# Performance work log

Hardware: AMD Instinct MI355X
Metric: run time of the kernel (lower is better)

Reference implementation:

```python
import jax, jax.numpy as jnp
import numpy as np

COMMITMENT_COST = 0.25
LAMBDA_KL = 1.0
EPS = 1e-10


def setup_inputs() -> dict:
    key = jax.random.key(0)
    k1, k2 = jax.random.split(key)
    x = jax.random.normal(k1, (8, 4096, 256), dtype=jnp.float32)
    embedding = jax.random.normal(k2, (1024, 256), dtype=jnp.float32)
    return {"x": x, "embedding": embedding}


def reference(x, embedding):
    B, T, D = x.shape
    M, _ = embedding.shape
    x_sg = jax.lax.stop_gradient(x)
    x_flat = x_sg.reshape(-1, D)  # [N, D]
    distances = (jnp.sum(embedding ** 2, axis=1)[None, :]
                 + jnp.sum(x_flat ** 2, axis=1, keepdims=True)
                 - 2.0 * (x_flat @ embedding.T))  # [N, M]
    indices = jnp.argmin(distances.astype(jnp.float32), axis=-1)  # [N]
    quantized = embedding[indices].reshape(B, T, D)
    # losses (x detached in both terms, matching torch)
    loss = (COMMITMENT_COST * jnp.mean((x_sg - quantized) ** 2)
            + jnp.mean((quantized - x_sg) ** 2)) * LAMBDA_KL
    # straight-through estimator
    quantized_st = x + jax.lax.stop_gradient(quantized - x)
    # avg of one-hot encodings == normalized code counts (avoids NxM one-hot)
    N = B * T
    counts = jnp.zeros((M,), dtype=jnp.float32).at[indices].add(1.0)
    avg_probs = counts / N
    perplexity = jnp.exp(-jnp.sum(avg_probs * jnp.log(avg_probs + EPS)))
    return (quantized_st, loss, indices.reshape(B, T), perplexity)
```

## Files before the change

### kernel.cpp

```cpp
#include <hip/hip_runtime.h>


constexpr int D = 256;
constexpr int M = 1024;
constexpr int SLICES = 4;
constexpr int CHUNK = 32;
constexpr int RPB = 512;

typedef _Float16 f16;
typedef __attribute__((ext_vector_type(4))) _Float16 f16x4;
typedef __attribute__((ext_vector_type(8))) _Float16 f16x8;
typedef __attribute__((ext_vector_type(4))) float f32x4;
typedef unsigned long long u64;
typedef unsigned int u32;

constexpr size_t WS_ENORM_F = 1028;
constexpr size_t WS_KEYS_B  = 16384;

__device__ inline u64 makekey(float v, int idx) {
    u32 b = __float_as_uint(v);
    u32 enc = (b & 0x80000000u) ? ~b : (b | 0x80000000u);
    return ((u64)enc << 32) | (u32)idx;
}

__global__ __launch_bounds__(512, 2) void vq_dist_kernel(
    const float* __restrict__ x, const float* __restrict__ e,
    u64* __restrict__ keys, float* __restrict__ ws, int groups)
{
    __shared__ ushort xH[2][CHUNK * D];
    __shared__ ushort xL[2][CHUNK * D];
    __shared__ u64    wred[8][CHUNK];

    const int tid = threadIdx.x;
    const int w  = __builtin_amdgcn_readfirstlane(tid >> 6);
    const int l  = tid & 63;
    const int lr = l & 15;
    const int q  = l >> 4;
    const int bswz = (lr & 7) << 4;

    const int slice = blockIdx.x / groups;
    const int group = blockIdx.x % groups;
    const int grow0 = group * RPB;
    const int ebase = slice * 256 + w * 32;

    f16x8 Ah[2][8], Al[2][8];
    float enR[2];
#pragma unroll
    for (int rf = 0; rf < 2; ++rf) {
        float sq = 0.f;
#pragma unroll
        for (int kk = 0; kk < 8; ++kk) {
            const float* p = e + (size_t)(ebase + rf * 16 + lr) * D + kk * 32 + q * 8;
            f32x4 a = *reinterpret_cast<const f32x4*>(p);
            f32x4 b = *reinterpret_cast<const f32x4*>(p + 4);
            f16 h0=(f16)a.x,h1=(f16)a.y,h2=(f16)a.z,h3=(f16)a.w;
            f16 h4=(f16)b.x,h5=(f16)b.y,h6=(f16)b.z,h7=(f16)b.w;
            Ah[rf][kk] = (f16x8){h0,h1,h2,h3,h4,h5,h6,h7};
            Al[rf][kk] = (f16x8){(f16)(a.x-(float)h0),(f16)(a.y-(float)h1),
                                 (f16)(a.z-(float)h2),(f16)(a.w-(float)h3),
                                 (f16)(b.x-(float)h4),(f16)(b.y-(float)h5),
                                 (f16)(b.z-(float)h6),(f16)(b.w-(float)h7)};
            sq = fmaf(a.x,a.x,fmaf(a.y,a.y,fmaf(a.z,a.z,fmaf(a.w,a.w,
                 fmaf(b.x,b.x,fmaf(b.y,b.y,fmaf(b.z,b.z,fmaf(b.w,b.w,sq))))))));
        }
        sq += __shfl_xor(sq, 16, 64);
        sq += __shfl_xor(sq, 32, 64);
        enR[rf] = sq;
    }
    float enA[2][4];
#pragma unroll
    for (int rf = 0; rf < 2; ++rf)
#pragma unroll
        for (int i = 0; i < 4; ++i)
            enA[rf][i] = __shfl(enR[rf], (l & 48) | (q * 4 + i), 64);

    float sxx = 0.f;
    f32x4 st[4];
#pragma unroll
    for (int i = 0; i < 4; ++i) {
        int f = i * 512 + tid, rr = f >> 6, c4 = f & 63;
        st[i] = *reinterpret_cast<const f32x4*>(x + (size_t)(grow0 + rr) * D + c4 * 4);
    }
    auto stage_write = [&](int nb) {
#pragma unroll
        for (int i = 0; i < 4; ++i) {
            int f = i * 512 + tid, rr = f >> 6, c4 = f & 63;
            f32x4 v = st[i];
            sxx = fmaf(v.x,v.x,fmaf(v.y,v.y,fmaf(v.z,v.z,fmaf(v.w,v.w,sxx))));
            f16 h0=(f16)v.x,h1=(f16)v.y,h2=(f16)v.z,h3=(f16)v.w;
            int byte = (rr * 512 + c4 * 8) ^ ((rr & 7) << 4);
            *reinterpret_cast<f16x4*>((char*)&xH[nb][0] + byte) = (f16x4){h0,h1,h2,h3};
            *reinterpret_cast<f16x4*>((char*)&xL[nb][0] + byte) =
                (f16x4){(f16)(v.x-(float)h0),(f16)(v.y-(float)h1),
                        (f16)(v.z-(float)h2),(f16)(v.w-(float)h3)};
        }
    };
    stage_write(0);

    const int nch = RPB / CHUNK;
    for (int c = 0; c < nch; ++c) {
        if (c + 1 < nch) {
#pragma unroll
            for (int i = 0; i < 4; ++i) {
                int f = i * 512 + tid, rr = f >> 6, c4 = f & 63;
                st[i] = *reinterpret_cast<const f32x4*>(
                    x + (size_t)(grow0 + (c + 1) * CHUNK + rr) * D + c4 * 4);
            }
        }
        __syncthreads();
        const int cb = c & 1;

        f32x4 acc[2][2];
#pragma unroll
        for (int rf = 0; rf < 2; ++rf)
#pragma unroll
            for (int cf = 0; cf < 2; ++cf) acc[rf][cf] = (f32x4){0.f,0.f,0.f,0.f};

#pragma unroll
        for (int kk = 0; kk < 8; ++kk) {
            f16x8 Bh[2], Bl[2];
#pragma unroll
            for (int cf = 0; cf < 2; ++cf) {
                int byte = ((cf * 16 + lr) * 512 + kk * 64 + q * 16) ^ bswz;
                Bh[cf] = *reinterpret_cast<const f16x8*>((const char*)&xH[cb][0] + byte);
                Bl[cf] = *reinterpret_cast<const f16x8*>((const char*)&xL[cb][0] + byte);
            }
#pragma unroll
            for (int rf = 0; rf < 2; ++rf)
#pragma unroll
                for (int cf = 0; cf < 2; ++cf) {
                    acc[rf][cf] = __builtin_amdgcn_mfma_f32_16x16x32_f16(Ah[rf][kk], Bh[cf], acc[rf][cf], 0, 0, 0);
                    acc[rf][cf] = __builtin_amdgcn_mfma_f32_16x16x32_f16(Ah[rf][kk], Bl[cf], acc[rf][cf], 0, 0, 0);
                    acc[rf][cf] = __builtin_amdgcn_mfma_f32_16x16x32_f16(Al[rf][kk], Bh[cf], acc[rf][cf], 0, 0, 0);
                }
        }

        float bV[2] = {3.4e38f, 3.4e38f};
        int   bI[2] = {0, 0};
#pragma unroll
        for (int rf = 0; rf < 2; ++rf)
#pragma unroll
            for (int i = 0; i < 4; ++i) {
                int   mi = ebase + rf * 16 + q * 4 + i;
                float en = enA[rf][i];
#pragma unroll
                for (int cf = 0; cf < 2; ++cf) {
                    float dv = fmaf(-2.f, acc[rf][cf][i], en);
                    if (dv < bV[cf]) { bV[cf] = dv; bI[cf] = mi; }
                }
            }
#pragma unroll
        for (int cf = 0; cf < 2; ++cf) {
#pragma unroll
            for (int mk = 16; mk <= 32; mk <<= 1) {
                float ov = __shfl_xor(bV[cf], mk, 64);
                int   oi = __shfl_xor(bI[cf], mk, 64);
                if (ov < bV[cf] || (ov == bV[cf] && oi < bI[cf])) { bV[cf] = ov; bI[cf] = oi; }
            }
        }
        if (q == 0) {
            wred[w][lr]      = makekey(bV[0], bI[0]);
            wred[w][16 + lr] = makekey(bV[1], bI[1]);
        }
        __syncthreads();

        if (tid < 32) {
            u64 k = wred[0][tid];
#pragma unroll
            for (int ww = 1; ww < 8; ++ww) { u64 k2 = wred[ww][tid]; k = (k2 < k) ? k2 : k; }
            atomicMin(&keys[grow0 + c * CHUNK + tid], k);
        }
        if (c + 1 < nch) stage_write((c + 1) & 1);
    }

    if (slice == 0) {
#pragma unroll
        for (int o = 32; o > 0; o >>= 1) sxx += __shfl_down(sxx, o, 64);
        if (l == 0) atomicAdd(ws, sxx);
    }
}

__global__ __launch_bounds__(256) void vq_gather_kernel(
    const float* __restrict__ e, const u64* __restrict__ keys,
    float* __restrict__ outQ, float* __restrict__ outIdx, float* __restrict__ ws)
{
    __shared__ int fidx[64];
    const int tid = threadIdx.x, row0 = blockIdx.x * 64;
    if (tid < 64) {
        u64 k = keys[row0 + tid];
        u32 enc = (u32)(k >> 32);
        u32 bits = (enc & 0x80000000u) ? (enc & 0x7fffffffu) : ~enc;
        float bv = __uint_as_float(bits);
        int idx = (int)(u32)(k & 0xffffffffu);
        fidx[tid] = idx;
        outIdx[row0 + tid] = (float)idx;
        atomicAdd(ws + 1 + idx, 1.0f);
        float s = bv;
#pragma unroll
        for (int o = 32; o > 0; o >>= 1) s += __shfl_down(s, o, 64);
        if (tid == 0) atomicAdd(ws, s);
    }
    __syncthreads();
#pragma unroll
    for (int it = 0; it < 16; ++it) {
        int f = it * 256 + tid, rr = f >> 6, c4 = f & 63;
        f32x4 v = *reinterpret_cast<const f32x4*>(e + (size_t)fidx[rr] * D + c4 * 4);
        __builtin_nontemporal_store(v, reinterpret_cast<f32x4*>(outQ + (size_t)(row0 + rr) * D + c4 * 4));
    }
}

__global__ void enorm_kernel(const float* __restrict__ e, float* __restrict__ enorm) {
    int m = blockIdx.x, l = threadIdx.x;
    const f32x4 v = *reinterpret_cast<const f32x4*>(e + m * D + l * 4);
    float s = fmaf(v.x, v.x, fmaf(v.y, v.y, fmaf(v.z, v.z, v.w * v.w)));
#pragma unroll
    for (int o = 32; o > 0; o >>= 1) s += __shfl_down(s, o, 64);
    if (l == 0) enorm[m] = s;
}

__global__ __launch_bounds__(256, 2) void vq_main_kernel(
    const float* __restrict__ x, const float* __restrict__ e,
    float* __restrict__ outQ, float* __restrict__ outIdx, float* __restrict__ ws) {
    __shared__ f32x4 xs[64][64];
    __shared__ float cval[4][64];
    __shared__ int   cidx[4][64];
    __shared__ int   fidx[64];
    const int tid = threadIdx.x, row0 = blockIdx.x * 64;
#pragma unroll
    for (int it = 0; it < 16; ++it) {
        int f = it * 256 + tid, rr = f >> 6, c4 = f & 63;
        xs[rr][c4 ^ (rr & 7)] = *reinterpret_cast<const f32x4*>(x + (row0 + rr) * D + c4 * 4);
    }
    __syncthreads();
    const int r = tid & 63, c = __builtin_amdgcn_readfirstlane(tid >> 6), sw = r & 7;
    float xnorm = 0.f;
    if (c == 0) {
        f32x4 a = (f32x4){0.f,0.f,0.f,0.f};
        for (int d4 = 0; d4 < 64; ++d4) {
            f32x4 xv = xs[r][d4 ^ sw];
            a.x = fmaf(xv.x, xv.x, a.x); a.y = fmaf(xv.y, xv.y, a.y);
            a.z = fmaf(xv.z, xv.z, a.z); a.w = fmaf(xv.w, xv.w, a.w);
        }
        xnorm = (a.x + a.y) + (a.z + a.w);
    }
    const float* __restrict__ enorm = ws + WS_ENORM_F;
    float bestVal = 3.4e38f; int bestIdx = 0;
    for (int chunk = 0; chunk < M / 32; ++chunk) {
        const int m0 = chunk * 32 + c * 8;
        f32x4 acc[8];
#pragma unroll
        for (int mi = 0; mi < 8; ++mi) acc[mi] = (f32x4){0.f,0.f,0.f,0.f};
#pragma unroll 2
        for (int d4 = 0; d4 < 64; ++d4) {
            const f32x4 xv = xs[r][d4 ^ sw];
#pragma unroll
            for (int mi = 0; mi < 8; ++mi) {
                const f32x4 ev = *reinterpret_cast<const f32x4*>(e + (m0 + mi) * D + d4 * 4);
                acc[mi].x = fmaf(xv.x, ev.x, acc[mi].x); acc[mi].y = fmaf(xv.y, ev.y, acc[mi].y);
                acc[mi].z = fmaf(xv.z, ev.z, acc[mi].z); acc[mi].w = fmaf(xv.w, ev.w, acc[mi].w);
            }
        }
#pragma unroll
        for (int mi = 0; mi < 8; ++mi) {
            float dot = (acc[mi].x + acc[mi].y) + (acc[mi].z + acc[mi].w);
            float val = enorm[m0 + mi] - 2.0f * dot;
            if (val < bestVal) { bestVal = val; bestIdx = m0 + mi; }
        }
    }
    cval[c][r] = bestVal; cidx[c][r] = bestIdx;
    __syncthreads();
    if (c == 0) {
        float bv = bestVal; int bi = bestIdx;
#pragma unroll
        for (int cc = 1; cc < 4; ++cc) {
            float v = cval[cc][r]; int i = cidx[cc][r];
            if (v < bv || (v == bv && i < bi)) { bv = v; bi = i; }
        }
        fidx[r] = bi; outIdx[row0 + r] = (float)bi;
        atomicAdd(ws + 1 + bi, 1.0f);
        float dist = bv + xnorm;
#pragma unroll
        for (int o = 32; o > 0; o >>= 1) dist += __shfl_down(dist, o, 64);
        if (r == 0) atomicAdd(ws, dist);
    }
    __syncthreads();
#pragma unroll
    for (int it = 0; it < 16; ++it) {
        int f = it * 256 + tid, rr = f >> 6, c4 = f & 63;
        *reinterpret_cast<f32x4*>(outQ + (row0 + rr) * D + c4 * 4) =
            *reinterpret_cast<const f32x4*>(e + fidx[rr] * D + c4 * 4);
    }
}

__global__ void vq_final_kernel(const float* __restrict__ ws,
                                float* __restrict__ outLoss, float* __restrict__ outPpl,
                                float invN, float invND) {
    int t = threadIdx.x;
    float p = ws[1 + t] * invN;
    float term = p * logf(p + 1e-10f);
#pragma unroll
    for (int o = 32; o > 0; o >>= 1) term += __shfl_down(term, o, 64);
    __shared__ float s[16];
    if ((t & 63) == 0) s[t >> 6] = term;
    __syncthreads();
    if (t == 0) {
        float tot = 0.f;
#pragma unroll
        for (int i = 0; i < 16; ++i) tot += s[i];
        *outPpl  = expf(-tot);
        *outLoss = 1.25f * ws[0] * invND;
    }
}

extern "C" void kernel_launch(void* const* d_in, const int* in_sizes, int n_in,
                              void* d_out, int out_size, void* d_ws, size_t ws_size,
                              hipStream_t stream) {
    const float* x = (const float*)d_in[0];
    const float* e = (const float*)d_in[1];
    const int NX = in_sizes[0];
    const int N  = NX / D;

    float* out     = (float*)d_out;
    float* outQ    = out;
    float* outLoss = out + NX;
    float* outIdx  = out + NX + 1;
    float* outPpl  = out + NX + 1 + N;
    float* ws      = (float*)d_ws;
    u64*   keys    = (u64*)((char*)d_ws + WS_KEYS_B);

    const size_t need = WS_KEYS_B + (size_t)N * 8;
    (void)hipMemsetAsync(d_ws, 0, 4100, stream);
    if (ws_size >= need && (N % RPB) == 0) {
        (void)hipMemsetAsync(keys, 0xFF, (size_t)N * 8, stream);
        const int groups = N / RPB;
        vq_dist_kernel<<<SLICES * groups, 512, 0, stream>>>(x, e, keys, ws, groups);
        vq_gather_kernel<<<N / 64, 256, 0, stream>>>(e, keys, outQ, outIdx, ws);
    } else {
        enorm_kernel<<<M, 64, 0, stream>>>(e, ws + WS_ENORM_F);
        vq_main_kernel<<<N / 64, 256, 0, stream>>>(x, e, outQ, outIdx, ws);
    }
    vq_final_kernel<<<1, 1024, 0, stream>>>(ws, outLoss, outPpl,
                                            1.0f / (float)N, 1.0f / (float)NX);
}
```

Baseline: 97.21 us.

## Fuse distance, argmin and gather with x-stationary tiles and prepacked codebook

Replaces the codebook-sliced distance kernel, the 64-bit key atomicMin buffer and the separate gather kernel with one fused kernel. In the new kernel each block keeps its 128 x rows as split-fp16 fragments in registers and streams a prepacked hi/lo fp16 codebook through double-buffered LDS using global_load_lds. A new prep kernel builds the packed codebook and its norms once per call. This removes the key memset, the atomics and a kernel launch, and the argmin is done fully in-register. The cost is that every block rereads the whole 1 MB packed codebook, and the grid is small (N/128 = 256 blocks).

Measured after the change: 93.71 us. -3.6%, faster.

```diff
diff --git a/kernel.cpp b/kernel.cpp
--- a/kernel.cpp
+++ b/kernel.cpp
@@ -3,209 +3,184 @@
 
 constexpr int D = 256;
 constexpr int M = 1024;
-constexpr int SLICES = 4;
-constexpr int CHUNK = 32;
-constexpr int RPB = 512;
 
 typedef _Float16 f16;
-typedef __attribute__((ext_vector_type(4))) _Float16 f16x4;
 typedef __attribute__((ext_vector_type(8))) _Float16 f16x8;
 typedef __attribute__((ext_vector_type(4))) float f32x4;
-typedef unsigned long long u64;
-typedef unsigned int u32;
 
 constexpr size_t WS_ENORM_F = 1028;
-constexpr size_t WS_KEYS_B  = 16384;
-
-__device__ inline u64 makekey(float v, int idx) {
-    u32 b = __float_as_uint(v);
-    u32 enc = (b & 0x80000000u) ? ~b : (b | 0x80000000u);
-    return ((u64)enc << 32) | (u32)idx;
-}
-
-__global__ __launch_bounds__(512, 2) void vq_dist_kernel(
+constexpr size_t WS_TAB_B   = 8320;
+constexpr size_t WS_NEEDED  = 1056896;
+
+__device__ inline void gload_lds16(const void* g, void* l) {
+    __builtin_amdgcn_global_load_lds(
+        (const __attribute__((address_space(1))) unsigned int*)(g),
+        (__attribute__((address_space(3))) unsigned int*)(l), 16, 0, 0);
+}
+
+__global__ __launch_bounds__(256) void prep_kernel(const float* __restrict__ e,
+                                                   float* __restrict__ ws) {
+    const int b = blockIdx.x, t = threadIdx.x;
+    if (b < 256) {
+        int v    = b * 256 + t;
+        int lane = v & 63, unit = v >> 6;
+        int rf = unit & 1, spl = (unit >> 1) & 1, kk = (unit >> 2) & 7, tile = unit >> 5;
+        int lr = lane & 15, q = lane >> 4;
+        const float* p = e + (size_t)(tile * 32 + rf * 16 + lr) * D + kk * 32 + q * 8;
+        f32x4 a = *reinterpret_cast<const f32x4*>(p);
+        f32x4 c = *reinterpret_cast<const f32x4*>(p + 4);
+        f16 h0=(f16)a.x,h1=(f16)a.y,h2=(f16)a.z,h3=(f16)a.w;
+        f16 h4=(f16)c.x,h5=(f16)c.y,h6=(f16)c.z,h7=(f16)c.w;
+        f16x8 out;
+        if (spl == 0) out = (f16x8){h0,h1,h2,h3,h4,h5,h6,h7};
+        else          out = (f16x8){(f16)(a.x-(float)h0),(f16)(a.y-(float)h1),
+                                    (f16)(a.z-(float)h2),(f16)(a.w-(float)h3),
+                                    (f16)(c.x-(float)h4),(f16)(c.y-(float)h5),
+                                    (f16)(c.z-(float)h6),(f16)(c.w-(float)h7)};
+        *reinterpret_cast<f16x8*>((char*)ws + WS_TAB_B + (size_t)v * 16) = out;
+    } else {
+        int row  = (b - 256) * 4 + (t >> 6);
+        int lane = t & 63;
+        f32x4 a = *reinterpret_cast<const f32x4*>(e + (size_t)row * D + lane * 4);
+        float s = fmaf(a.x, a.x, fmaf(a.y, a.y, fmaf(a.z, a.z, a.w * a.w)));
+#pragma unroll
+        for (int o = 32; o > 0; o >>= 1) s += __shfl_down(s, o, 64);
+        if (lane == 0) ws[WS_ENORM_F + row] = s;
+    }
+}
+
+__global__ __launch_bounds__(256, 2) void vq_fused_kernel(
     const float* __restrict__ x, const float* __restrict__ e,
-    u64* __restrict__ keys, float* __restrict__ ws, int groups)
+    float* __restrict__ outQ, float* __restrict__ outIdx, float* __restrict__ ws)
 {
-    __shared__ ushort xH[2][CHUNK * D];
-    __shared__ ushort xL[2][CHUNK * D];
-    __shared__ u64    wred[8][CHUNK];
+    __shared__ ushort ebuf[2][16384];
+    __shared__ float  en_s[M];
+    __shared__ int    fidx[128];
+    __shared__ float  lsum[4];
 
     const int tid = threadIdx.x;
-    const int w  = __builtin_amdgcn_readfirstlane(tid >> 6);
-    const int l  = tid & 63;
-    const int lr = l & 15;
-    const int q  = l >> 4;
-    const int bswz = (lr & 7) << 4;
-
-    const int slice = blockIdx.x / groups;
-    const int group = blockIdx.x % groups;
-    const int grow0 = group * RPB;
-    const int ebase = slice * 256 + w * 32;
-
-    f16x8 Ah[2][8], Al[2][8];
-    float enR[2];
-#pragma unroll
-    for (int rf = 0; rf < 2; ++rf) {
-        float sq = 0.f;
+    const int w   = __builtin_amdgcn_readfirstlane(tid >> 6);
+    const int l   = tid & 63;
+    const int lr  = l & 15, q = l >> 4;
+    const int R   = blockIdx.x * 128;
+    const char* tab = (const char*)ws + WS_TAB_B;
+
+    {
+        f32x4 v = *reinterpret_cast<const f32x4*>(ws + WS_ENORM_F + tid * 4);
+        *reinterpret_cast<f32x4*>(&en_s[tid * 4]) = v;
+    }
+
+    f16x8 Xh[2][8], Xl[2][8];
+    float xn[2];
+#pragma unroll
+    for (int cf = 0; cf < 2; ++cf) {
+        float s = 0.f;
 #pragma unroll
         for (int kk = 0; kk < 8; ++kk) {
-            const float* p = e + (size_t)(ebase + rf * 16 + lr) * D + kk * 32 + q * 8;
+            const float* p = x + (size_t)(R + w * 32 + cf * 16 + lr) * D + kk * 32 + q * 8;
             f32x4 a = *reinterpret_cast<const f32x4*>(p);
-            f32x4 b = *reinterpret_cast<const f32x4*>(p + 4);
+            f32x4 c = *reinterpret_cast<const f32x4*>(p + 4);
             f16 h0=(f16)a.x,h1=(f16)a.y,h2=(f16)a.z,h3=(f16)a.w;
-            f16 h4=(f16)b.x,h5=(f16)b.y,h6=(f16)b.z,h7=(f16)b.w;
-            Ah[rf][kk] = (f16x8){h0,h1,h2,h3,h4,h5,h6,h7};
-            Al[rf][kk] = (f16x8){(f16)(a.x-(float)h0),(f16)(a.y-(float)h1),
+            f16 h4=(f16)c.x,h5=(f16)c.y,h6=(f16)c.z,h7=(f16)c.w;
+            Xh[cf][kk] = (f16x8){h0,h1,h2,h3,h4,h5,h6,h7};
+            Xl[cf][kk] = (f16x8){(f16)(a.x-(float)h0),(f16)(a.y-(float)h1),
                                  (f16)(a.z-(float)h2),(f16)(a.w-(float)h3),
-                                 (f16)(b.x-(float)h4),(f16)(b.y-(float)h5),
-                                 (f16)(b.z-(float)h6),(f16)(b.w-(float)h7)};
-            sq = fmaf(a.x,a.x,fmaf(a.y,a.y,fmaf(a.z,a.z,fmaf(a.w,a.w,
-                 fmaf(b.x,b.x,fmaf(b.y,b.y,fmaf(b.z,b.z,fmaf(b.w,b.w,sq))))))));
-        }
-        sq += __shfl_xor(sq, 16, 64);
-        sq += __shfl_xor(sq, 32, 64);
-        enR[rf] = sq;
-    }
-    float enA[2][4];
-#pragma unroll
-    for (int rf = 0; rf < 2; ++rf)
-#pragma unroll
-        for (int i = 0; i < 4; ++i)
-            enA[rf][i] = __shfl(enR[rf], (l & 48) | (q * 4 + i), 64);
-
-    float sxx = 0.f;
-    f32x4 st[4];
-#pragma unroll
-    for (int i = 0; i < 4; ++i) {
-        int f = i * 512 + tid, rr = f >> 6, c4 = f & 63;
-        st[i] = *reinterpret_cast<const f32x4*>(x + (size_t)(grow0 + rr) * D + c4 * 4);
-    }
-    auto stage_write = [&](int nb) {
-#pragma unroll
-        for (int i = 0; i < 4; ++i) {
-            int f = i * 512 + tid, rr = f >> 6, c4 = f & 63;
-            f32x4 v = st[i];
-            sxx = fmaf(v.x,v.x,fmaf(v.y,v.y,fmaf(v.z,v.z,fmaf(v.w,v.w,sxx))));
-            f16 h0=(f16)v.x,h1=(f16)v.y,h2=(f16)v.z,h3=(f16)v.w;
-            int byte = (rr * 512 + c4 * 8) ^ ((rr & 7) << 4);
-            *reinterpret_cast<f16x4*>((char*)&xH[nb][0] + byte) = (f16x4){h0,h1,h2,h3};
-            *reinterpret_cast<f16x4*>((char*)&xL[nb][0] + byte) =
-                (f16x4){(f16)(v.x-(float)h0),(f16)(v.y-(float)h1),
-                        (f16)(v.z-(float)h2),(f16)(v.w-(float)h3)};
-        }
-    };
-    stage_write(0);
-
-    const int nch = RPB / CHUNK;
-    for (int c = 0; c < nch; ++c) {
-        if (c + 1 < nch) {
+                                 (f16)(c.x-(float)h4),(f16)(c.y-(float)h5),
+                                 (f16)(c.z-(float)h6),(f16)(c.w-(float)h7)};
+            s = fmaf(a.x,a.x,fmaf(a.y,a.y,fmaf(a.z,a.z,fmaf(a.w,a.w,
+                fmaf(c.x,c.x,fmaf(c.y,c.y,fmaf(c.z,c.z,fmaf(c.w,c.w,s))))))));
+        }
+        s += __shfl_xor(s, 16, 64);
+        s += __shfl_xor(s, 32, 64);
+        xn[cf] = s;
+    }
+
+#pragma unroll
+    for (int i = 0; i < 8; ++i)
+        gload_lds16(tab + (w * 8 + i) * 1024 + l * 16, &ebuf[0][(w * 8 + i) * 512]);
+    __syncthreads();
+
+    float bV[2] = {3.4e38f, 3.4e38f};
+    int   bI[2] = {0, 0};
+
+    for (int t = 0; t < 32; ++t) {
+        const ushort* eb = &ebuf[t & 1][0];
+        if (t < 31) {
+            const char* gt = tab + (size_t)(t + 1) * 32768;
+            ushort* lb = &ebuf[(t + 1) & 1][0];
+#pragma unroll
+            for (int i = 0; i < 8; ++i)
+                gload_lds16(gt + (w * 8 + i) * 1024 + l * 16, lb + (w * 8 + i) * 512);
+        }
+
+        f32x4 acc[2][2];
+#pragma unroll
+        for (int rf = 0; rf < 2; ++rf)
+#pragma unroll
+            for (int cf = 0; cf < 2; ++cf) acc[rf][cf] = (f32x4){0.f,0.f,0.f,0.f};
+
+#pragma unroll
+        for (int kk = 0; kk < 8; ++kk) {
+            f16x8 Ah0 = *reinterpret_cast<const f16x8*>(eb + (kk*4+0)*512 + l*8);
+            f16x8 Ah1 = *reinterpret_cast<const f16x8*>(eb + (kk*4+1)*512 + l*8);
+            f16x8 Al0 = *reinterpret_cast<const f16x8*>(eb + (kk*4+2)*512 + l*8);
+            f16x8 Al1 = *reinterpret_cast<const f16x8*>(eb + (kk*4+3)*512 + l*8);
+#pragma unroll
+            for (int cf = 0; cf < 2; ++cf) {
+                acc[0][cf] = __builtin_amdgcn_mfma_f32_16x16x32_f16(Ah0, Xh[cf][kk], acc[0][cf], 0, 0, 0);
+                acc[0][cf] = __builtin_amdgcn_mfma_f32_16x16x32_f16(Ah0, Xl[cf][kk], acc[0][cf], 0, 0, 0);
+                acc[0][cf] = __builtin_amdgcn_mfma_f32_16x16x32_f16(Al0, Xh[cf][kk], acc[0][cf], 0, 0, 0);
+                acc[1][cf] = __builtin_amdgcn_mfma_f32_16x16x32_f16(Ah1, Xh[cf][kk], acc[1][cf], 0, 0, 0);
+                acc[1][cf] = __builtin_amdgcn_mfma_f32_16x16x32_f16(Ah1, Xl[cf][kk], acc[1][cf], 0, 0, 0);
+                acc[1][cf] = __builtin_amdgcn_mfma_f32_16x16x32_f16(Al1, Xh[cf][kk], acc[1][cf], 0, 0, 0);
+            }
+        }
+
+#pragma unroll
+        for (int rf = 0; rf < 2; ++rf)
 #pragma unroll
             for (int i = 0; i < 4; ++i) {
-                int f = i * 512 + tid, rr = f >> 6, c4 = f & 63;
-                st[i] = *reinterpret_cast<const f32x4*>(
-                    x + (size_t)(grow0 + (c + 1) * CHUNK + rr) * D + c4 * 4);
-            }
-        }
-        __syncthreads();
-        const int cb = c & 1;
-
-        f32x4 acc[2][2];
-#pragma unroll
-        for (int rf = 0; rf < 2; ++rf)
-#pragma unroll
-            for (int cf = 0; cf < 2; ++cf) acc[rf][cf] = (f32x4){0.f,0.f,0.f,0.f};
-
-#pragma unroll
-        for (int kk = 0; kk < 8; ++kk) {
-            f16x8 Bh[2], Bl[2];
-#pragma unroll
-            for (int cf = 0; cf < 2; ++cf) {
-                int byte = ((cf * 16 + lr) * 512 + kk * 64 + q * 16) ^ bswz;
-                Bh[cf] = *reinterpret_cast<const f16x8*>((const char*)&xH[cb][0] + byte);
-                Bl[cf] = *reinterpret_cast<const f16x8*>((const char*)&xL[cb][0] + byte);
-            }
-#pragma unroll
-            for (int rf = 0; rf < 2; ++rf)
-#pragma unroll
-                for (int cf = 0; cf < 2; ++cf) {
-                    acc[rf][cf] = __builtin_amdgcn_mfma_f32_16x16x32_f16(Ah[rf][kk], Bh[cf], acc[rf][cf], 0, 0, 0);
-                    acc[rf][cf] = __builtin_amdgcn_mfma_f32_16x16x32_f16(Ah[rf][kk], Bl[cf], acc[rf][cf], 0, 0, 0);
-                    acc[rf][cf] = __builtin_amdgcn_mfma_f32_16x16x32_f16(Al[rf][kk], Bh[cf], acc[rf][cf], 0, 0, 0);
-                }
-        }
-
-        float bV[2] = {3.4e38f, 3.4e38f};
-        int   bI[2] = {0, 0};
-#pragma unroll
-        for (int rf = 0; rf < 2; ++rf)
-#pragma unroll
-            for (int i = 0; i < 4; ++i) {
-                int   mi = ebase + rf * 16 + q * 4 + i;
-                float en = enA[rf][i];
+                int   mi = t * 32 + rf * 16 + q * 4 + i;
+                float en = en_s[mi];
 #pragma unroll
                 for (int cf = 0; cf < 2; ++cf) {
                     float dv = fmaf(-2.f, acc[rf][cf][i], en);
                     if (dv < bV[cf]) { bV[cf] = dv; bI[cf] = mi; }
                 }
             }
-#pragma unroll
-        for (int cf = 0; cf < 2; ++cf) {
-#pragma unroll
-            for (int mk = 16; mk <= 32; mk <<= 1) {
-                float ov = __shfl_xor(bV[cf], mk, 64);
-                int   oi = __shfl_xor(bI[cf], mk, 64);
-                if (ov < bV[cf] || (ov == bV[cf] && oi < bI[cf])) { bV[cf] = ov; bI[cf] = oi; }
-            }
-        }
-        if (q == 0) {
-            wred[w][lr]      = makekey(bV[0], bI[0]);
-            wred[w][16 + lr] = makekey(bV[1], bI[1]);
-        }
         __syncthreads();
-
-        if (tid < 32) {
-            u64 k = wred[0][tid];
-#pragma unroll
-            for (int ww = 1; ww < 8; ++ww) { u64 k2 = wred[ww][tid]; k = (k2 < k) ? k2 : k; }
-            atomicMin(&keys[grow0 + c * CHUNK + tid], k);
-        }
-        if (c + 1 < nch) stage_write((c + 1) & 1);
-    }
-
-    if (slice == 0) {
-#pragma unroll
-        for (int o = 32; o > 0; o >>= 1) sxx += __shfl_down(sxx, o, 64);
-        if (l == 0) atomicAdd(ws, sxx);
-    }
-}
-
-__global__ __launch_bounds__(256) void vq_gather_kernel(
-    const float* __restrict__ e, const u64* __restrict__ keys,
-    float* __restrict__ outQ, float* __restrict__ outIdx, float* __restrict__ ws)
-{
-    __shared__ int fidx[64];
-    const int tid = threadIdx.x, row0 = blockIdx.x * 64;
-    if (tid < 64) {
-        u64 k = keys[row0 + tid];
-        u32 enc = (u32)(k >> 32);
-        u32 bits = (enc & 0x80000000u) ? (enc & 0x7fffffffu) : ~enc;
-        float bv = __uint_as_float(bits);
-        int idx = (int)(u32)(k & 0xffffffffu);
-        fidx[tid] = idx;
-        outIdx[row0 + tid] = (float)idx;
-        atomicAdd(ws + 1 + idx, 1.0f);
-        float s = bv;
-#pragma unroll
-        for (int o = 32; o > 0; o >>= 1) s += __shfl_down(s, o, 64);
-        if (tid == 0) atomicAdd(ws, s);
-    }
-    __syncthreads();
-#pragma unroll
-    for (int it = 0; it < 16; ++it) {
-        int f = it * 256 + tid, rr = f >> 6, c4 = f & 63;
-        f32x4 v = *reinterpret_cast<const f32x4*>(e + (size_t)fidx[rr] * D + c4 * 4);
-        __builtin_nontemporal_store(v, reinterpret_cast<f32x4*>(outQ + (size_t)(row0 + rr) * D + c4 * 4));
+    }
+
+#pragma unroll
+    for (int cf = 0; cf < 2; ++cf) {
+#pragma unroll
+        for (int mk = 16; mk <= 32; mk <<= 1) {
+            float ov = __shfl_xor(bV[cf], mk, 64);
+            int   oi = __shfl_xor(bI[cf], mk, 64);
+            if (ov < bV[cf] || (ov == bV[cf] && oi < bI[cf])) { bV[cf] = ov; bI[cf] = oi; }
+        }
+    }
+    if (q == 0) {
+        fidx[w * 32 + lr]      = bI[0];
+        fidx[w * 32 + 16 + lr] = bI[1];
+        outIdx[R + w * 32 + lr]      = (float)bI[0];
+        outIdx[R + w * 32 + 16 + lr] = (float)bI[1];
+        atomicAdd(ws + 1 + bI[0], 1.0f);
+        atomicAdd(ws + 1 + bI[1], 1.0f);
+        float ls = bV[0] + bV[1] + xn[0] + xn[1];
+#pragma unroll
+        for (int o = 8; o > 0; o >>= 1) ls += __shfl_down(ls, o, 64);
+        if (lr == 0) lsum[w] = ls;
+    }
+    __syncthreads();
+    if (tid == 0) atomicAdd(ws, lsum[0] + lsum[1] + lsum[2] + lsum[3]);
+
+#pragma unroll
+    for (int it = 0; it < 32; ++it) {
+        int u = it * 256 + tid;
+        int row = u >> 6, c4 = u & 63;
+        f32x4 v = *reinterpret_cast<const f32x4*>(e + (size_t)fidx[row] * D + c4 * 4);
+        __builtin_nontemporal_store(v, reinterpret_cast<f32x4*>(outQ + (size_t)(R + row) * D + c4 * 4));
     }
 }
 
@@ -326,15 +301,11 @@
     float* outIdx  = out + NX + 1;
     float* outPpl  = out + NX + 1 + N;
     float* ws      = (float*)d_ws;
-    u64*   keys    = (u64*)((char*)d_ws + WS_KEYS_B);
-
-    const size_t need = WS_KEYS_B + (size_t)N * 8;
+
     (void)hipMemsetAsync(d_ws, 0, 4100, stream);
-    if (ws_size >= need && (N % RPB) == 0) {
-        (void)hipMemsetAsync(keys, 0xFF, (size_t)N * 8, stream);
-        const int groups = N / RPB;
-        vq_dist_kernel<<<SLICES * groups, 512, 0, stream>>>(x, e, keys, ws, groups);
-        vq_gather_kernel<<<N / 64, 256, 0, stream>>>(e, keys, outQ, outIdx, ws);
+    if (ws_size >= WS_NEEDED && (N % 128) == 0) {
+        prep_kernel<<<512, 256, 0, stream>>>(e, ws);
+        vq_fused_kernel<<<N / 128, 256, 0, stream>>>(x, e, outQ, outIdx, ws);
     } else {
         enorm_kernel<<<M, 64, 0, stream>>>(e, ws + WS_ENORM_F);
         vq_main_kernel<<<N / 64, 256, 0, stream>>>(x, e, outQ, outIdx, ws);
```
